# Kernel tuning notes

Hardware: AMD Instinct MI355X
Metric: run time of the kernel (lower is better)

## Reference

```python
import jax, jax.numpy as jnp
import numpy as np

VOCAB = 200000
HID = 128
OUT = 5
N_LEAVES = 512  # balanced tree -> 1023 total nodes, children precede parents


def _build_tree(n_leaves):
    n = 2 * n_leaves - 1
    left = np.zeros(n, dtype=np.int32)
    right = np.zeros(n, dtype=np.int32)
    is_leaf = np.zeros(n, dtype=bool)
    is_leaf[:n_leaves] = True
    level = list(range(n_leaves))
    idx = n_leaves
    while len(level) > 1:
        nxt = []
        for a, b in zip(level[::2], level[1::2]):
            left[idx] = a
            right[idx] = b
            nxt.append(idx)
            idx += 1
        level = nxt
    return left, right, is_leaf


def setup_inputs() -> dict:
    key = jax.random.key(0)
    ks = jax.random.split(key, 7)
    left, right, is_leaf = _build_tree(N_LEAVES)
    n = left.shape[0]
    word_ids = jax.random.randint(ks[0], (n,), 0, VOCAB, dtype=jnp.int32)
    s = 0.05  # small init scale to keep tanh un-saturated; math identical
    return {
        "embed": jax.random.normal(ks[1], (VOCAB, HID), jnp.float32) * s,
        "V": jax.random.normal(ks[2], (HID, 2 * HID, 2 * HID), jnp.float32) * s,
        "W": jax.random.normal(ks[3], (2 * HID, HID), jnp.float32) * s,
        "b": jax.random.normal(ks[4], (1, HID), jnp.float32) * s,
        "W_out_w": jax.random.normal(ks[5], (OUT, HID), jnp.float32) * s,
        "W_out_b": jax.random.normal(ks[6], (OUT,), jnp.float32) * s,
        "word_ids": word_ids,
        "left": jnp.asarray(left),
        "right": jnp.asarray(right),
        "is_leaf": jnp.asarray(is_leaf),
    }


def reference(embed, V, W, b, W_out_w, W_out_b, word_ids, left, right, is_leaf):
    n = word_ids.shape[0]
    h = embed.shape[1]
    H0 = jnp.zeros((n, h), dtype=embed.dtype)

    def step(H, inp):
        t, wid, l, r, leaf = inp

        def leaf_fn():
            return embed[wid]

        def internal_fn():
            x = jnp.concatenate([H[l], H[r]])  # (2h,) concated child states
            # torch loop over V slices == einsum over stacked V: (x V_k x^T)_k
            xVx = jnp.einsum('i,kij,j->k', x, V, x)
            return jnp.tanh(xVx + x @ W + b[0])

        cur = jax.lax.cond(leaf, leaf_fn, internal_fn)
        return H.at[t].set(cur), None

    xs = (jnp.arange(n), word_ids, left, right, is_leaf)
    H, _ = jax.lax.scan(step, H0, xs)
    logits = H @ W_out_w.T + W_out_b
    return jax.nn.log_softmax(logits, axis=1)
```

## Files before the change

### kernel.cpp

```cpp
#include <hip/hip_runtime.h>
#include <math.h>

#define HID 128
#define DD 256
#define NNODES 1023
#define NLEAVES 512

typedef __attribute__((ext_vector_type(8))) short short8;
typedef __attribute__((ext_vector_type(4))) float f32x4;

__device__ __forceinline__ unsigned short f2bf(float f) {
    unsigned int u = __float_as_uint(f);
    u += 0x7FFFu + ((u >> 16) & 1u);
    return (unsigned short)(u >> 16);
}
__device__ __forceinline__ float bf2f(unsigned short s) {
    return __uint_as_float(((unsigned int)s) << 16);
}
__device__ __forceinline__ void pack_hilo(float a, float c, unsigned& h, unsigned& l) {
    const unsigned short ha = f2bf(a), hc = f2bf(c);
    const unsigned short la = f2bf(a - bf2f(ha)), lc = f2bf(c - bf2f(hc));
    h = (unsigned)ha | ((unsigned)hc << 16);
    l = (unsigned)la | ((unsigned)lc << 16);
}

__global__ void conv_kernel(const float* __restrict__ V,
                            unsigned short* __restrict__ Vh,
                            unsigned short* __restrict__ Vl) {
    const size_t t = (size_t)blockIdx.x * 256 + threadIdx.x;
    const float4 a = ((const float4*)V)[2 * t];
    const float4 c = ((const float4*)V)[2 * t + 1];
    uint4 ph, pl;
    pack_hilo(a.x, a.y, ph.x, pl.x);
    pack_hilo(a.z, a.w, ph.y, pl.y);
    pack_hilo(c.x, c.y, ph.z, pl.z);
    pack_hilo(c.z, c.w, ph.w, pl.w);
    ((uint4*)Vh)[t] = ph;
    ((uint4*)Vl)[t] = pl;
}

__global__ void leaf_kernel(const float* __restrict__ embed,
                            const int* __restrict__ word_ids,
                            float* __restrict__ H) {
    const int t = blockIdx.x;
    const int h = threadIdx.x;
    H[(size_t)t * HID + h] = embed[(size_t)word_ids[t] * HID + h];
}

template<int MT, int GX>
__global__ __launch_bounds__(256)
void level_mfma(const unsigned short* __restrict__ Vh, const unsigned short* __restrict__ Vl,
                const float* __restrict__ W, const float* __restrict__ b,
                const int* __restrict__ left, const int* __restrict__ right,
                float* __restrict__ H, int levelStart, int nn) {
    constexpr int ROWS = MT * 16;
    __shared__ __align__(16) unsigned short Xh[ROWS * 256];
    __shared__ __align__(16) unsigned short Xl[ROWS * 256];
    __shared__ float qred[ROWS * 4];

    const int t = threadIdx.x;
    const int orig = blockIdx.x + GX * blockIdx.y;
    const int vid = (orig & 7) * ((GX * 128) >> 3) + (orig >> 3);
    const int k = vid / GX;
    const int n0 = (vid % GX) * ROWS;

    for (int idx = t; idx < ROWS * 32; idx += 256) {
        const int row = idx >> 5;
        const int i0 = (idx & 31) * 8;
        const int n = n0 + row;
        uint4 ph = make_uint4(0u, 0u, 0u, 0u), pl = ph;
        if (n < nn) {
            const int node = levelStart + n;
            const int child = (i0 < HID) ? left[node] : right[node];
            const float4* hp = (const float4*)&H[(size_t)child * HID + (i0 & 127)];
            const float4 x0 = hp[0], x1 = hp[1];
            pack_hilo(x0.x, x0.y, ph.x, pl.x);
            pack_hilo(x0.z, x0.w, ph.y, pl.y);
            pack_hilo(x1.x, x1.y, ph.z, pl.z);
            pack_hilo(x1.z, x1.w, ph.w, pl.w);
        }
        const int ad = (row * 256 + i0) ^ ((row & 7) << 3);
        *(uint4*)&Xh[ad] = ph;
        *(uint4*)&Xl[ad] = pl;
    }
    __syncthreads();

    const int w = t >> 6;
    const int lane = t & 63;
    const int colsel = lane & 15;
    const int kg = lane >> 4;
    const int ibase = w * 64;

    f32x4 acc[MT][4];
#pragma unroll
    for (int m = 0; m < MT; ++m)
#pragma unroll
        for (int it = 0; it < 4; ++it) acc[m][it] = (f32x4){0.f, 0.f, 0.f, 0.f};

    const size_t vkb = ((size_t)k << 16);

#pragma unroll
    for (int ks = 0; ks < 8; ++ks) {
        const int jb = ks * 32 + kg * 8;
        short8 ah[MT], al[MT];
#pragma unroll
        for (int m = 0; m < MT; ++m) {
            const int row = m * 16 + colsel;
            const int ad = (row * 256 + jb) ^ ((row & 7) << 3);
            ah[m] = *(const short8*)&Xh[ad];
            al[m] = *(const short8*)&Xl[ad];
        }
#pragma unroll
        for (int it = 0; it < 4; ++it) {
            const int icol = ibase + it * 16 + colsel;
            const size_t vo = vkb + (size_t)icol * 256 + jb;
            const short8 bh = *(const short8*)&Vh[vo];
            const short8 bl = *(const short8*)&Vl[vo];
#pragma unroll
            for (int m = 0; m < MT; ++m)
                acc[m][it] = __builtin_amdgcn_mfma_f32_16x16x32_bf16(ah[m], bh, acc[m][it], 0, 0, 0);
#pragma unroll
            for (int m = 0; m < MT; ++m)
                acc[m][it] = __builtin_amdgcn_mfma_f32_16x16x32_bf16(al[m], bh, acc[m][it], 0, 0, 0);
#pragma unroll
            for (int m = 0; m < MT; ++m)
                acc[m][it] = __builtin_amdgcn_mfma_f32_16x16x32_bf16(ah[m], bl, acc[m][it], 0, 0, 0);
        }
    }

    float q[MT][4];
#pragma unroll
    for (int m = 0; m < MT; ++m)
#pragma unroll
        for (int r = 0; r < 4; ++r) q[m][r] = 0.f;

#pragma unroll
    for (int it = 0; it < 4; ++it) {
        const int ig = ibase + it * 16 + colsel;
        const float wv = W[(size_t)ig * HID + k];
#pragma unroll
        for (int m = 0; m < MT; ++m) {
#pragma unroll
            for (int r = 0; r < 4; ++r) {
                const int row = m * 16 + kg * 4 + r;
                const int ad = (row * 256 + ig) ^ ((row & 7) << 3);
                const float xv = bf2f(Xh[ad]) + bf2f(Xl[ad]);
                q[m][r] = fmaf(xv, acc[m][it][r] + wv, q[m][r]);
            }
        }
    }
#pragma unroll
    for (int m = 0; m < MT; ++m)
#pragma unroll
        for (int r = 0; r < 4; ++r)
#pragma unroll
            for (int msk = 1; msk < 16; msk <<= 1)
                q[m][r] += __shfl_xor(q[m][r], msk, 64);

    if (colsel == 0) {
#pragma unroll
        for (int m = 0; m < MT; ++m)
#pragma unroll
            for (int r = 0; r < 4; ++r)
                qred[(m * 16 + kg * 4 + r) * 4 + w] = q[m][r];
    }
    __syncthreads();
    if (t < ROWS) {
        const int n = n0 + t;
        if (n < nn) {
            const float s = b[k] + qred[t * 4 + 0] + qred[t * 4 + 1]
                                 + qred[t * 4 + 2] + qred[t * 4 + 3];
            H[(size_t)(levelStart + n) * HID + k] = tanhf(s);
        }
    }
}

__global__ void out_kernel(const float* __restrict__ H,
                           const float* __restrict__ Wout,
                           const float* __restrict__ bout,
                           float* __restrict__ out) {
    const int t = blockIdx.x;
    const int l = threadIdx.x;
    const float h0 = H[(size_t)t * HID + l];
    const float h1 = H[(size_t)t * HID + 64 + l];
    float p[5];
#pragma unroll
    for (int o = 0; o < 5; ++o) {
        p[o] = h0 * Wout[o * HID + l] + h1 * Wout[o * HID + 64 + l];
#pragma unroll
        for (int m = 1; m < 64; m <<= 1) p[o] += __shfl_xor(p[o], m, 64);
    }
    if (l == 0) {
        float lg[5], mx = -1e30f;
#pragma unroll
        for (int o = 0; o < 5; ++o) { lg[o] = p[o] + bout[o]; mx = fmaxf(mx, lg[o]); }
        float s = 0.f;
#pragma unroll
        for (int o = 0; o < 5; ++o) s += expf(lg[o] - mx);
        const float lse = mx + logf(s);
#pragma unroll
        for (int o = 0; o < 5; ++o) out[(size_t)t * 5 + o] = lg[o] - lse;
    }
}

extern "C" void kernel_launch(void* const* d_in, const int* in_sizes, int n_in,
                              void* d_out, int out_size, void* d_ws, size_t ws_size,
                              hipStream_t stream) {
    const float* embed   = (const float*)d_in[0];
    const float* V       = (const float*)d_in[1];
    const float* W       = (const float*)d_in[2];
    const float* b       = (const float*)d_in[3];
    const float* Woutw   = (const float*)d_in[4];
    const float* Woutb   = (const float*)d_in[5];
    const int*   wordids = (const int*)d_in[6];
    const int*   left    = (const int*)d_in[7];
    const int*   right   = (const int*)d_in[8];

    const size_t VSZ = (size_t)128 * 256 * 256;
    unsigned short* Vbh = (unsigned short*)d_ws;
    unsigned short* Vbl = Vbh + VSZ;
    float* H   = (float*)((char*)d_ws + 4 * VSZ);
    float* out = (float*)d_out;

    conv_kernel<<<4096, 256, 0, stream>>>(V, Vbh, Vbl);
    leaf_kernel<<<NLEAVES, HID, 0, stream>>>(embed, wordids, H);

    level_mfma<4,4><<<dim3(4,128), 256, 0, stream>>>(Vbh, Vbl, W, b, left, right, H, 512, 256);
    level_mfma<4,2><<<dim3(2,128), 256, 0, stream>>>(Vbh, Vbl, W, b, left, right, H, 768, 128);
    level_mfma<4,1><<<dim3(1,128), 256, 0, stream>>>(Vbh, Vbl, W, b, left, right, H, 896,  64);
    level_mfma<2,1><<<dim3(1,128), 256, 0, stream>>>(Vbh, Vbl, W, b, left, right, H, 960,  32);
    level_mfma<1,1><<<dim3(1,128), 256, 0, stream>>>(Vbh, Vbl, W, b, left, right, H, 992,  16);
    level_mfma<1,1><<<dim3(1,128), 256, 0, stream>>>(Vbh, Vbl, W, b, left, right, H, 1008,  8);
    level_mfma<1,1><<<dim3(1,128), 256, 0, stream>>>(Vbh, Vbl, W, b, left, right, H, 1016,  4);
    level_mfma<1,1><<<dim3(1,128), 256, 0, stream>>>(Vbh, Vbl, W, b, left, right, H, 1020,  2);
    level_mfma<1,1><<<dim3(1,128), 256, 0, stream>>>(Vbh, Vbl, W, b, left, right, H, 1022,  1);

    out_kernel<<<NNODES, 64, 0, stream>>>(H, Woutw, Woutb, out);
}
```

Before: 311.5 us.

## Pre-swizzle V into MFMA fragment layout and give each block two k-slices

```diff
diff --git a/kernel.cpp b/kernel.cpp
--- a/kernel.cpp
+++ b/kernel.cpp
@@ -2,11 +2,11 @@
 #include <math.h>
 
 #define HID 128
-#define DD 256
 #define NNODES 1023
 #define NLEAVES 512
 
 typedef __attribute__((ext_vector_type(8))) short short8;
+typedef __attribute__((ext_vector_type(4))) short short4v;
 typedef __attribute__((ext_vector_type(4))) float f32x4;
 
 __device__ __forceinline__ unsigned short f2bf(float f) {
@@ -24,50 +24,66 @@
     l = (unsigned)la | ((unsigned)lc << 16);
 }
 
-__global__ void conv_kernel(const float* __restrict__ V,
-                            unsigned short* __restrict__ Vh,
-                            unsigned short* __restrict__ Vl) {
-    const size_t t = (size_t)blockIdx.x * 256 + threadIdx.x;
-    const float4 a = ((const float4*)V)[2 * t];
-    const float4 c = ((const float4*)V)[2 * t + 1];
-    uint4 ph, pl;
-    pack_hilo(a.x, a.y, ph.x, pl.x);
-    pack_hilo(a.z, a.w, ph.y, pl.y);
-    pack_hilo(c.x, c.y, ph.z, pl.z);
-    pack_hilo(c.z, c.w, ph.w, pl.w);
-    ((uint4*)Vh)[t] = ph;
-    ((uint4*)Vl)[t] = pl;
+__global__ void conv_kernel(const float* __restrict__ V, const float* __restrict__ W,
+                            unsigned short* __restrict__ Vp, float* __restrict__ Wt) {
+    const int ihalf = blockIdx.x, k = blockIdx.y;
+    const int t = threadIdx.x, w = t >> 6, lane = t & 63;
+    const int colsel = lane & 15, kg = lane >> 4;
+    const size_t srcK = (size_t)k << 16;
+    const size_t dstK = (size_t)k << 17;
+#pragma unroll
+    for (int fi = 0; fi < 16; ++fi) {
+        const int frag = w * 16 + fi, ks = frag >> 3, it = frag & 7;
+        const int irow = ihalf * 128 + it * 16 + colsel;
+        const int j0 = ks * 32 + kg * 8;
+        const float4 s0 = *(const float4*)&V[srcK + (size_t)irow * 256 + j0];
+        const float4 s1 = *(const float4*)&V[srcK + (size_t)irow * 256 + j0 + 4];
+        uint4 ph, pl;
+        pack_hilo(s0.x, s0.y, ph.x, pl.x);
+        pack_hilo(s0.z, s0.w, ph.y, pl.y);
+        pack_hilo(s1.x, s1.y, ph.z, pl.z);
+        pack_hilo(s1.z, s1.w, ph.w, pl.w);
+        const size_t d = dstK + (size_t)((ihalf * 8 + ks) * 8 + it) * 1024 + lane * 8;
+        *(uint4*)&Vp[d] = ph;
+        *(uint4*)&Vp[d + 512] = pl;
+    }
+    if (ihalf == 0) Wt[(size_t)k * 256 + t] = W[(size_t)t * HID + k];
 }
 
 __global__ void leaf_kernel(const float* __restrict__ embed,
                             const int* __restrict__ word_ids,
                             float* __restrict__ H) {
-    const int t = blockIdx.x;
-    const int h = threadIdx.x;
+    const int t = blockIdx.x, h = threadIdx.x;
     H[(size_t)t * HID + h] = embed[(size_t)word_ids[t] * HID + h];
 }
 
-template<int MT, int GX>
-__global__ __launch_bounds__(256)
-void level_mfma(const unsigned short* __restrict__ Vh, const unsigned short* __restrict__ Vl,
-                const float* __restrict__ W, const float* __restrict__ b,
-                const int* __restrict__ left, const int* __restrict__ right,
-                float* __restrict__ H, int levelStart, int nn) {
-    constexpr int ROWS = MT * 16;
+template<int NR>
+__global__ __launch_bounds__(256, 2)
+void level_mfma(const unsigned short* __restrict__ Vp, const float* __restrict__ Wt,
+                const float* __restrict__ b, const int* __restrict__ left,
+                const int* __restrict__ right, float* __restrict__ H,
+                int levelStart, int nn) {
+    constexpr int ROWS = NR * 16;
     __shared__ __align__(16) unsigned short Xh[ROWS * 256];
     __shared__ __align__(16) unsigned short Xl[ROWS * 256];
-    __shared__ float qred[ROWS * 4];
+    __shared__ float qred[2 * 64 * 2];
 
     const int t = threadIdx.x;
-    const int orig = blockIdx.x + GX * blockIdx.y;
-    const int vid = (orig & 7) * ((GX * 128) >> 3) + (orig >> 3);
-    const int k = vid / GX;
-    const int n0 = (vid % GX) * ROWS;
+    const int fl = blockIdx.x + gridDim.x * blockIdx.y;
+    const int gX = gridDim.x;
+    const int xcd = fl & 7, r2 = fl >> 3;
+    const int gxv = r2 % gX;
+    const int gyv = xcd * 8 + r2 / gX;
+    const int k0 = gyv * 2;
+    const int w = t >> 6, lane = t & 63;
+    const int kslot = w >> 1, ihalf = w & 1;
+    const int k = k0 + kslot;
+    const int colsel = lane & 15, kg = lane >> 4;
+    const size_t kbase = (size_t)k << 17;
+    const int n0 = gxv * ROWS;
 
     for (int idx = t; idx < ROWS * 32; idx += 256) {
-        const int row = idx >> 5;
-        const int i0 = (idx & 31) * 8;
-        const int n = n0 + row;
+        const int row = idx >> 5, i0 = (idx & 31) * 8, n = n0 + row;
         uint4 ph = make_uint4(0u, 0u, 0u, 0u), pl = ph;
         if (n < nn) {
             const int node = levelStart + n;
@@ -85,92 +101,74 @@
     }
     __syncthreads();
 
-    const int w = t >> 6;
-    const int lane = t & 63;
-    const int colsel = lane & 15;
-    const int kg = lane >> 4;
-    const int ibase = w * 64;
-
-    f32x4 acc[MT][4];
-#pragma unroll
-    for (int m = 0; m < MT; ++m)
-#pragma unroll
-        for (int it = 0; it < 4; ++it) acc[m][it] = (f32x4){0.f, 0.f, 0.f, 0.f};
-
-    const size_t vkb = ((size_t)k << 16);
+    f32x4 acc[NR][8];
+#pragma unroll
+    for (int it = 0; it < 8; ++it) {
+        const f32x4 wv = *(const f32x4*)&Wt[(size_t)k * 256 + ihalf * 128 + it * 16 + kg * 4];
+#pragma unroll
+        for (int nr = 0; nr < NR; ++nr) acc[nr][it] = wv;
+    }
 
 #pragma unroll
     for (int ks = 0; ks < 8; ++ks) {
-        const int jb = ks * 32 + kg * 8;
-        short8 ah[MT], al[MT];
-#pragma unroll
-        for (int m = 0; m < MT; ++m) {
-            const int row = m * 16 + colsel;
-            const int ad = (row * 256 + jb) ^ ((row & 7) << 3);
-            ah[m] = *(const short8*)&Xh[ad];
-            al[m] = *(const short8*)&Xl[ad];
-        }
-#pragma unroll
-        for (int it = 0; it < 4; ++it) {
-            const int icol = ibase + it * 16 + colsel;
-            const size_t vo = vkb + (size_t)icol * 256 + jb;
-            const short8 bh = *(const short8*)&Vh[vo];
-            const short8 bl = *(const short8*)&Vl[vo];
-#pragma unroll
-            for (int m = 0; m < MT; ++m)
-                acc[m][it] = __builtin_amdgcn_mfma_f32_16x16x32_bf16(ah[m], bh, acc[m][it], 0, 0, 0);
-#pragma unroll
-            for (int m = 0; m < MT; ++m)
-                acc[m][it] = __builtin_amdgcn_mfma_f32_16x16x32_bf16(al[m], bh, acc[m][it], 0, 0, 0);
-#pragma unroll
-            for (int m = 0; m < MT; ++m)
-                acc[m][it] = __builtin_amdgcn_mfma_f32_16x16x32_bf16(ah[m], bl, acc[m][it], 0, 0, 0);
-        }
-    }
-
-    float q[MT][4];
-#pragma unroll
-    for (int m = 0; m < MT; ++m)
-#pragma unroll
-        for (int r = 0; r < 4; ++r) q[m][r] = 0.f;
-
-#pragma unroll
-    for (int it = 0; it < 4; ++it) {
-        const int ig = ibase + it * 16 + colsel;
-        const float wv = W[(size_t)ig * HID + k];
-#pragma unroll
-        for (int m = 0; m < MT; ++m) {
+        short8 xh[NR], xl[NR];
+#pragma unroll
+        for (int nr = 0; nr < NR; ++nr) {
+            const int row = nr * 16 + colsel;
+            const int ad = (row * 256 + ks * 32 + kg * 8) ^ ((row & 7) << 3);
+            xh[nr] = *(const short8*)&Xh[ad];
+            xl[nr] = *(const short8*)&Xl[ad];
+        }
+        const size_t fb = kbase + (size_t)((ihalf * 8 + ks) * 8) * 1024 + lane * 8;
+#pragma unroll
+        for (int it = 0; it < 8; ++it) {
+            const short8 vh = *(const short8*)&Vp[fb + it * 1024];
+            const short8 vl = *(const short8*)&Vp[fb + it * 1024 + 512];
+#pragma unroll
+            for (int nr = 0; nr < NR; ++nr) {
+                acc[nr][it] = __builtin_amdgcn_mfma_f32_16x16x32_bf16(vh, xh[nr], acc[nr][it], 0, 0, 0);
+                acc[nr][it] = __builtin_amdgcn_mfma_f32_16x16x32_bf16(vl, xh[nr], acc[nr][it], 0, 0, 0);
+                acc[nr][it] = __builtin_amdgcn_mfma_f32_16x16x32_bf16(vh, xl[nr], acc[nr][it], 0, 0, 0);
+            }
+        }
+    }
+
+    float qp[NR];
+#pragma unroll
+    for (int nr = 0; nr < NR; ++nr) qp[nr] = 0.f;
+#pragma unroll
+    for (int it = 0; it < 8; ++it) {
+        const int i0 = ihalf * 128 + it * 16 + kg * 4;
+#pragma unroll
+        for (int nr = 0; nr < NR; ++nr) {
+            const int row = nr * 16 + colsel;
+            const int ad = (row * 256 + i0) ^ ((row & 7) << 3);
+            const short4v h4 = *(const short4v*)&Xh[ad];
+            const short4v l4 = *(const short4v*)&Xl[ad];
 #pragma unroll
             for (int r = 0; r < 4; ++r) {
-                const int row = m * 16 + kg * 4 + r;
-                const int ad = (row * 256 + ig) ^ ((row & 7) << 3);
-                const float xv = bf2f(Xh[ad]) + bf2f(Xl[ad]);
-                q[m][r] = fmaf(xv, acc[m][it][r] + wv, q[m][r]);
+                const float x = bf2f((unsigned short)h4[r]) + bf2f((unsigned short)l4[r]);
+                qp[nr] = fmaf(x, acc[nr][it][r], qp[nr]);
             }
         }
     }
 #pragma unroll
-    for (int m = 0; m < MT; ++m)
-#pragma unroll
-        for (int r = 0; r < 4; ++r)
-#pragma unroll
-            for (int msk = 1; msk < 16; msk <<= 1)
-                q[m][r] += __shfl_xor(q[m][r], msk, 64);
-
-    if (colsel == 0) {
-#pragma unroll
-        for (int m = 0; m < MT; ++m)
-#pragma unroll
-            for (int r = 0; r < 4; ++r)
-                qred[(m * 16 + kg * 4 + r) * 4 + w] = q[m][r];
+    for (int nr = 0; nr < NR; ++nr) {
+        qp[nr] += __shfl_xor(qp[nr], 16, 64);
+        qp[nr] += __shfl_xor(qp[nr], 32, 64);
+    }
+    if (kg == 0) {
+#pragma unroll
+        for (int nr = 0; nr < NR; ++nr)
+            qred[(kslot * 64 + nr * 16 + colsel) * 2 + ihalf] = qp[nr];
     }
     __syncthreads();
-    if (t < ROWS) {
-        const int n = n0 + t;
-        if (n < nn) {
-            const float s = b[k] + qred[t * 4 + 0] + qred[t * 4 + 1]
-                                 + qred[t * 4 + 2] + qred[t * 4 + 3];
-            H[(size_t)(levelStart + n) * HID + k] = tanhf(s);
+    if (t < 128) {
+        const int ksl = t >> 6, n = t & 63;
+        if (n < ROWS && n0 + n < nn) {
+            const float s = b[k0 + ksl] + qred[(ksl * 64 + n) * 2 + 0]
+                                        + qred[(ksl * 64 + n) * 2 + 1];
+            H[(size_t)(levelStart + n0 + n) * HID + (k0 + ksl)] = tanhf(s);
         }
     }
 }
@@ -179,8 +177,7 @@
                            const float* __restrict__ Wout,
                            const float* __restrict__ bout,
                            float* __restrict__ out) {
-    const int t = blockIdx.x;
-    const int l = threadIdx.x;
+    const int t = blockIdx.x, l = threadIdx.x;
     const float h0 = H[(size_t)t * HID + l];
     const float h1 = H[(size_t)t * HID + 64 + l];
     float p[5];
@@ -216,24 +213,23 @@
     const int*   left    = (const int*)d_in[7];
     const int*   right   = (const int*)d_in[8];
 
-    const size_t VSZ = (size_t)128 * 256 * 256;
-    unsigned short* Vbh = (unsigned short*)d_ws;
-    unsigned short* Vbl = Vbh + VSZ;
-    float* H   = (float*)((char*)d_ws + 4 * VSZ);
+    unsigned short* Vp = (unsigned short*)d_ws;
+    float* Wt  = (float*)((char*)d_ws + (size_t)128 * 131072 * 2);
+    float* H   = Wt + (size_t)128 * 256;
     float* out = (float*)d_out;
 
-    conv_kernel<<<4096, 256, 0, stream>>>(V, Vbh, Vbl);
+    conv_kernel<<<dim3(2, 128), 256, 0, stream>>>(V, W, Vp, Wt);
     leaf_kernel<<<NLEAVES, HID, 0, stream>>>(embed, wordids, H);
 
-    level_mfma<4,4><<<dim3(4,128), 256, 0, stream>>>(Vbh, Vbl, W, b, left, right, H, 512, 256);
-    level_mfma<4,2><<<dim3(2,128), 256, 0, stream>>>(Vbh, Vbl, W, b, left, right, H, 768, 128);
-    level_mfma<4,1><<<dim3(1,128), 256, 0, stream>>>(Vbh, Vbl, W, b, left, right, H, 896,  64);
-    level_mfma<2,1><<<dim3(1,128), 256, 0, stream>>>(Vbh, Vbl, W, b, left, right, H, 960,  32);
-    level_mfma<1,1><<<dim3(1,128), 256, 0, stream>>>(Vbh, Vbl, W, b, left, right, H, 992,  16);
-    level_mfma<1,1><<<dim3(1,128), 256, 0, stream>>>(Vbh, Vbl, W, b, left, right, H, 1008,  8);
-    level_mfma<1,1><<<dim3(1,128), 256, 0, stream>>>(Vbh, Vbl, W, b, left, right, H, 1016,  4);
-    level_mfma<1,1><<<dim3(1,128), 256, 0, stream>>>(Vbh, Vbl, W, b, left, right, H, 1020,  2);
-    level_mfma<1,1><<<dim3(1,128), 256, 0, stream>>>(Vbh, Vbl, W, b, left, right, H, 1022,  1);
+    level_mfma<4><<<dim3(4, 64), 256, 0, stream>>>(Vp, Wt, b, left, right, H, 512, 256);
+    level_mfma<4><<<dim3(2, 64), 256, 0, stream>>>(Vp, Wt, b, left, right, H, 768, 128);
+    level_mfma<4><<<dim3(1, 64), 256, 0, stream>>>(Vp, Wt, b, left, right, H, 896,  64);
+    level_mfma<2><<<dim3(1, 64), 256, 0, stream>>>(Vp, Wt, b, left, right, H, 960,  32);
+    level_mfma<1><<<dim3(1, 64), 256, 0, stream>>>(Vp, Wt, b, left, right, H, 992,  16);
+    level_mfma<1><<<dim3(1, 64), 256, 0, stream>>>(Vp, Wt, b, left, right, H, 1008,  8);
+    level_mfma<1><<<dim3(1, 64), 256, 0, stream>>>(Vp, Wt, b, left, right, H, 1016,  4);
+    level_mfma<1><<<dim3(1, 64), 256, 0, stream>>>(Vp, Wt, b, left, right, H, 1020,  2);
+    level_mfma<1><<<dim3(1, 64), 256, 0, stream>>>(Vp, Wt, b, left, right, H, 1022,  1);
 
     out_kernel<<<NNODES, 64, 0, stream>>>(H, Woutw, Woutb, out);
 }
```

Measured after the change: 343.7 us. +10.4%, slower.
